# Optimization experiments

Hardware: AMD Instinct MI355X
Metric: run time of the kernel (lower is better)

The kernel has to match this reference:

```python
import jax, jax.numpy as jnp
import numpy as np

D_IN = 1024
D_OUT = 1024
NUM_HEADS = 16
HEAD_DIM = D_OUT // NUM_HEADS
SEQ = 2048
BATCH = 4


def setup_inputs() -> dict:
    key = jax.random.key(0)
    ks = jax.random.split(key, 6)
    s_in = 1.0 / np.sqrt(D_IN)
    s_out = 1.0 / np.sqrt(D_OUT)
    return {
        "inputs": jax.random.normal(ks[0], (BATCH, SEQ, D_IN), dtype=jnp.float32),
        # nn.Linear stores weight as [out, in]; y = x @ W.T
        "W_q": jax.random.uniform(ks[1], (D_OUT, D_IN), jnp.float32, -s_in, s_in),
        "W_k": jax.random.uniform(ks[2], (D_OUT, D_IN), jnp.float32, -s_in, s_in),
        "W_v": jax.random.uniform(ks[3], (D_OUT, D_IN), jnp.float32, -s_in, s_in),
        "W_o": jax.random.uniform(ks[4], (D_OUT, D_OUT), jnp.float32, -s_out, s_out),
        "b_o": jax.random.uniform(ks[5], (D_OUT,), jnp.float32, -s_out, s_out),
    }


def reference(inputs, W_q, W_k, W_v, W_o, b_o):
    B, T, _ = inputs.shape
    # projections: [B, T, d_out] -> [B, H, T, hd]
    def split_heads(x):
        return x.reshape(B, T, NUM_HEADS, HEAD_DIM).transpose(0, 2, 1, 3)

    Q = split_heads(inputs @ W_q.T)
    K = split_heads(inputs @ W_k.T)
    V = split_heads(inputs @ W_v.T)

    # [B, H, T, T] causal attention scores
    scores = jnp.einsum("bhqd,bhkd->bhqk", Q, K)
    causal = jnp.tril(jnp.ones((T, T), dtype=bool))  # True = keep
    scores = jnp.where(causal, scores, -jnp.inf)
    weights = jax.nn.softmax(scores / np.sqrt(HEAD_DIM), axis=-1)
    # dropout p=0.0 (eval mode): identity

    ctx = jnp.einsum("bhqk,bhkd->bhqd", weights, V)
    ctx = ctx.transpose(0, 2, 1, 3).reshape(B, T, D_OUT)
    return ctx @ W_o.T + b_o
```

## Files before the change

kernel.cpp:

```cpp
#include <hip/hip_runtime.h>
#include <cstdint>
#include <cstddef>

#define D_MODEL 1024
#define SEQQ    2048
#define NBATCH  4
#define NHEAD   16
#define HDIM    64
#define MTOT    (NBATCH * SEQQ)

typedef __attribute__((ext_vector_type(8))) short short8;
typedef __attribute__((ext_vector_type(4))) float floatx4;
typedef unsigned short u16;

__device__ __forceinline__ u16 f2bf(float f) {
  union { float f; uint32_t u; } a; a.f = f;
  uint32_t u = a.u;
  u += 0x7fffu + ((u >> 16) & 1u);
  return (u16)(u >> 16);
}

__device__ __forceinline__ floatx4 mfma16(short8 a, short8 b, floatx4 c) {
  return __builtin_amdgcn_mfma_f32_16x16x32_bf16(a, b, c, 0, 0, 0);
}

__device__ __forceinline__ void load_lds16(const void* g, void* l) {
  __builtin_amdgcn_global_load_lds(
      (const __attribute__((address_space(1))) uint32_t*)g,
      (__attribute__((address_space(3))) uint32_t*)l, 16, 0, 0);
}

__global__ __launch_bounds__(256) void k_cast_all(
    const float* __restrict__ X, const float* __restrict__ w0,
    const float* __restrict__ w1, const float* __restrict__ w2,
    const float* __restrict__ w3,
    u16* __restrict__ xb, u16* __restrict__ y0, u16* __restrict__ y1,
    u16* __restrict__ y2, u16* __restrict__ y3) {
  const int bx = blockIdx.x;
  const float* src; u16* dst; int i;
  if (bx < 8192) {
    src = X; dst = xb; i = (bx * 256 + threadIdx.x) * 4;
  } else {
    const int w = (bx - 8192) >> 10;
    src = (w == 0) ? w0 : (w == 1) ? w1 : (w == 2) ? w2 : w3;
    dst = (w == 0) ? y0 : (w == 1) ? y1 : (w == 2) ? y2 : y3;
    i = (((bx - 8192) & 1023) * 256 + threadIdx.x) * 4;
  }
  float4 v = *(const float4*)(src + i);
  ushort4 o;
  o.x = f2bf(v.x); o.y = f2bf(v.y); o.z = f2bf(v.z); o.w = f2bf(v.w);
  *(ushort4*)(dst + i) = o;
}

__global__ __launch_bounds__(256) void k_gemm_bt(
    const u16* __restrict__ A,
    const u16* __restrict__ B0, const u16* __restrict__ B1, const u16* __restrict__ B2,
    void* __restrict__ C0, void* __restrict__ C1, u16* __restrict__ VtOut,
    const float* __restrict__ bias, int M, int N, int K, int f32out, float ascaleQ) {
  __shared__ __align__(16) u16 As[128 * 64];
  __shared__ __align__(16) u16 Bs[128 * 64];
  const int tid = threadIdx.x;
  const int lane = tid & 63, wave = tid >> 6;
  const int quad = lane >> 4, l15 = lane & 15;
  const int m0 = blockIdx.y * 128, n0 = blockIdx.x * 128;
  const int wr = wave >> 1, wc = wave & 1;
  const u16* Bm = (blockIdx.z == 0) ? B0 : (blockIdx.z == 1 ? B1 : B2);
  void* Cm = (blockIdx.z == 0) ? C0 : C1;
  const float ascale = (blockIdx.z == 0) ? ascaleQ : 1.0f;

  floatx4 acc[4][4];
#pragma unroll
  for (int i = 0; i < 4; ++i)
#pragma unroll
    for (int j = 0; j < 4; ++j) acc[i][j] = (floatx4){0.f, 0.f, 0.f, 0.f};

  const int srow = tid >> 3;
  const int scolx = ((tid & 7) * 8) ^ ((srow & 7) * 8);
  const u16* Ag = A + (size_t)(m0 + srow) * K + scolx;
  const u16* Bg = Bm + (size_t)(n0 + srow) * K + scolx;

  for (int kt = 0; kt < K; kt += 64) {
    __syncthreads();
#pragma unroll
    for (int p = 0; p < 4; ++p) {
      load_lds16(Ag + (size_t)(p * 32) * K + kt, &As[p * 2048 + wave * 512]);
      load_lds16(Bg + (size_t)(p * 32) * K + kt, &Bs[p * 2048 + wave * 512]);
    }
    __syncthreads();

    short8 af[2][4], bfg[2][4];
#pragma unroll
    for (int ks = 0; ks < 2; ++ks) {
      const int kkx = (ks * 32 + quad * 8) ^ ((l15 & 7) * 8);
#pragma unroll
      for (int i = 0; i < 4; ++i) {
        af[ks][i]  = *(const short8*)&As[(wr * 64 + i * 16 + l15) * 64 + kkx];
        bfg[ks][i] = *(const short8*)&Bs[(wc * 64 + i * 16 + l15) * 64 + kkx];
      }
    }
#pragma unroll
    for (int ks = 0; ks < 2; ++ks)
#pragma unroll
      for (int mi = 0; mi < 4; ++mi)
#pragma unroll
        for (int ni = 0; ni < 4; ++ni)
          acc[mi][ni] = mfma16(af[ks][mi], bfg[ks][ni], acc[mi][ni]);
  }

  if (blockIdx.z == 2) {
#pragma unroll
    for (int mi = 0; mi < 4; ++mi) {
#pragma unroll
      for (int ni = 0; ni < 4; ++ni) {
        const int row = m0 + wr * 64 + mi * 16 + quad * 4;
        const int col = n0 + wc * 64 + ni * 16 + l15;
        const int b = row >> 11, t = row & 2047;
        const int h = col >> 6, d = col & 63;
        ushort4 pk;
        pk.x = f2bf(acc[mi][ni][0]); pk.y = f2bf(acc[mi][ni][1]);
        pk.z = f2bf(acc[mi][ni][2]); pk.w = f2bf(acc[mi][ni][3]);
        *(ushort4*)(VtOut + (((size_t)(b * 16 + h) * 64 + d) * SEQQ + t)) = pk;
      }
    }
    return;
  }
#pragma unroll
  for (int mi = 0; mi < 4; ++mi) {
#pragma unroll
    for (int ni = 0; ni < 4; ++ni) {
      const int row = m0 + wr * 64 + mi * 16 + quad * 4;
      const int col = n0 + wc * 64 + ni * 16 + l15;
      const float bv = bias ? bias[col] : 0.f;
#pragma unroll
      for (int r = 0; r < 4; ++r) {
        const float v = acc[mi][ni][r] * ascale + bv;
        if (f32out) ((float*)Cm)[(size_t)(row + r) * N + col] = v;
        else        ((u16*)Cm)[(size_t)(row + r) * N + col] = f2bf(v);
      }
    }
  }
}

__device__ __forceinline__ void softmax_pack(
    floatx4 (&st)[4], float& lp, u16* psw, int quad, int l15) {
#pragma unroll
  for (int ni = 0; ni < 4; ++ni) {
    const float p0 = __builtin_amdgcn_exp2f(st[ni][0]);
    const float p1 = __builtin_amdgcn_exp2f(st[ni][1]);
    const float p2 = __builtin_amdgcn_exp2f(st[ni][2]);
    const float p3 = __builtin_amdgcn_exp2f(st[ni][3]);
    lp += (p0 + p1) + (p2 + p3);
    uint2 pk;
    pk.x = __builtin_amdgcn_perm(__float_as_uint(p1), __float_as_uint(p0), 0x07060302u);
    pk.y = __builtin_amdgcn_perm(__float_as_uint(p3), __float_as_uint(p2), 0x07060302u);
    *(uint2*)&psw[l15 * 64 + ((ni * 16 + quad * 4) ^ ((l15 & 7) * 8))] = pk;
  }
}

__device__ __forceinline__ void pv_mfma(
    floatx4 (&acc)[4], const u16* psw, const short8 (&vf)[2][4], int quad, int l15) {
#pragma unroll
  for (int kc = 0; kc < 2; ++kc) {
    const short8 pf = *(const short8*)&psw[l15 * 64 +
                                           ((kc * 32 + quad * 8) ^ ((l15 & 7) * 8))];
#pragma unroll
    for (int di = 0; di < 4; ++di)
      acc[di] = mfma16(pf, vf[kc][di], acc[di]);
  }
}

__global__ __launch_bounds__(256) void k_attn(
    const u16* __restrict__ Q, const u16* __restrict__ Kg,
    const u16* __restrict__ Vt, u16* __restrict__ O) {
  __shared__ __align__(16) u16 Ks[2][64 * 64];
  __shared__ __align__(16) u16 Vs[2][64 * 64];
  __shared__ __align__(16) u16 Ps[4][2][16 * 64];
  const int tid = threadIdx.x, lane = tid & 63, wave = tid >> 6;
  const int quad = lane >> 4, l15 = lane & 15;

  const int lin = blockIdx.x;
  const int kgrp = lin >> 8, c = lin & 255;
  const int a = c & 7;
  const int p = (kgrp & 1) ? (15 - a) : a;
  const int bh = ((c >> 3) << 1) | (kgrp >> 1);
  const int b = bh >> 4, h = bh & 15;

  const int qwA = 64 * p + wave * 16;
  const int qwB = SEQQ - 64 * (p + 1) + wave * 16;
  const int nT = 32 - p;

  const u16* kbase = Kg + (size_t)(b * SEQQ) * D_MODEL + h * HDIM;
  const u16* vbase = Vt + (size_t)bh * (HDIM * SEQQ);

  const int srow = tid >> 3;
  const int scol = ((tid & 7) * 8) ^ ((srow & 7) * 8);

  {
    load_lds16(kbase + (size_t)srow * D_MODEL + scol,        &Ks[0][wave * 512]);
    load_lds16(kbase + (size_t)(32 + srow) * D_MODEL + scol, &Ks[0][2048 + wave * 512]);
    load_lds16(vbase + (size_t)srow * SEQQ + scol,           &Vs[0][wave * 512]);
    load_lds16(vbase + (size_t)(32 + srow) * SEQQ + scol,    &Vs[0][2048 + wave * 512]);
  }

  short8 qfA[2], qfB[2];
  {
    const u16* qa = Q + (size_t)(b * SEQQ + qwA + l15) * D_MODEL + h * HDIM;
    const u16* qb = Q + (size_t)(b * SEQQ + qwB + l15) * D_MODEL + h * HDIM;
#pragma unroll
    for (int ks = 0; ks < 2; ++ks) {
      qfA[ks] = *(const short8*)(qa + ks * 32 + quad * 8);
      qfB[ks] = *(const short8*)(qb + ks * 32 + quad * 8);
    }
  }

  floatx4 accA[4], accB[4];
  float lAp = 0.f, lBp = 0.f;
#pragma unroll
  for (int i = 0; i < 4; ++i) {
    accA[i] = (floatx4){0.f, 0.f, 0.f, 0.f};
    accB[i] = (floatx4){0.f, 0.f, 0.f, 0.f};
  }

  u16* pswA = &Ps[wave][0][0];
  u16* pswB = &Ps[wave][1][0];

  for (int t = 0; t < nT; ++t) {
    const int cur = t & 1;
    __syncthreads();
    if (t + 1 < nT) {
      const int kt1 = (t + 1) * 64, nxt = cur ^ 1;
      load_lds16(kbase + (size_t)(kt1 + srow) * D_MODEL + scol,      &Ks[nxt][wave * 512]);
      load_lds16(kbase + (size_t)(kt1 + 32 + srow) * D_MODEL + scol, &Ks[nxt][2048 + wave * 512]);
      load_lds16(vbase + (size_t)srow * SEQQ + kt1 + scol,           &Vs[nxt][wave * 512]);
      load_lds16(vbase + (size_t)(32 + srow) * SEQQ + kt1 + scol,    &Vs[nxt][2048 + wave * 512]);
    }
    const int kt = t * 64;

    short8 kf[4][2];
#pragma unroll
    for (int ni = 0; ni < 4; ++ni)
#pragma unroll
      for (int ks = 0; ks < 2; ++ks)
        kf[ni][ks] = *(const short8*)&Ks[cur][(ni * 16 + l15) * 64 +
                                            ((ks * 32 + quad * 8) ^ ((l15 & 7) * 8))];
    short8 vf[2][4];
#pragma unroll
    for (int kc = 0; kc < 2; ++kc)
#pragma unroll
      for (int di = 0; di < 4; ++di)
        vf[kc][di] = *(const short8*)&Vs[cur][(di * 16 + l15) * 64 +
                                             ((kc * 32 + quad * 8) ^ ((l15 & 7) * 8))];

    const bool doA = (t <= p);
    if (doA) {
      floatx4 st[4];
#pragma unroll
      for (int ni = 0; ni < 4; ++ni) {
        floatx4 s = (floatx4){0.f, 0.f, 0.f, 0.f};
        s = mfma16(kf[ni][0], qfA[0], s);
        s = mfma16(kf[ni][1], qfA[1], s);
        st[ni] = s;
      }
      if (t == p) {
        const int qg = qwA + l15;
#pragma unroll
        for (int ni = 0; ni < 4; ++ni) {
          const int kg = kt + ni * 16 + quad * 4;
#pragma unroll
          for (int r = 0; r < 4; ++r)
            if (kg + r > qg) st[ni][r] = -1e30f;
        }
      }
      softmax_pack(st, lAp, pswA, quad, l15);
    }
    {
      floatx4 st[4];
#pragma unroll
      for (int ni = 0; ni < 4; ++ni) {
        floatx4 s = (floatx4){0.f, 0.f, 0.f, 0.f};
        s = mfma16(kf[ni][0], qfB[0], s);
        s = mfma16(kf[ni][1], qfB[1], s);
        st[ni] = s;
      }
      if (t == nT - 1) {
        const int qg = qwB + l15;
#pragma unroll
        for (int ni = 0; ni < 4; ++ni) {
          const int kg = kt + ni * 16 + quad * 4;
#pragma unroll
          for (int r = 0; r < 4; ++r)
            if (kg + r > qg) st[ni][r] = -1e30f;
        }
      }
      softmax_pack(st, lBp, pswB, quad, l15);
    }
    asm volatile("s_waitcnt lgkmcnt(0)" ::: "memory");
    if (doA) pv_mfma(accA, pswA, vf, quad, l15);
    pv_mfma(accB, pswB, vf, quad, l15);
  }

  lAp += __shfl_xor(lAp, 16); lAp += __shfl_xor(lAp, 32);
  lBp += __shfl_xor(lBp, 16); lBp += __shfl_xor(lBp, 32);

  {
    u16* orow = O + (size_t)(b * SEQQ + qwA + quad * 4) * D_MODEL + h * HDIM + l15;
#pragma unroll
    for (int r = 0; r < 4; ++r) {
      const float inv = 1.0f / __shfl(lAp, quad * 4 + r, 16);
#pragma unroll
      for (int di = 0; di < 4; ++di)
        orow[(size_t)r * D_MODEL + di * 16] = f2bf(accA[di][r] * inv);
    }
  }
  {
    u16* orow = O + (size_t)(b * SEQQ + qwB + quad * 4) * D_MODEL + h * HDIM + l15;
#pragma unroll
    for (int r = 0; r < 4; ++r) {
      const float inv = 1.0f / __shfl(lBp, quad * 4 + r, 16);
#pragma unroll
      for (int di = 0; di < 4; ++di)
        orow[(size_t)r * D_MODEL + di * 16] = f2bf(accB[di][r] * inv);
    }
  }
}

extern "C" void kernel_launch(void* const* d_in, const int* in_sizes, int n_in,
                              void* d_out, int out_size, void* d_ws, size_t ws_size,
                              hipStream_t stream) {
  const float* X  = (const float*)d_in[0];
  const float* Wq = (const float*)d_in[1];
  const float* Wk = (const float*)d_in[2];
  const float* Wv = (const float*)d_in[3];
  const float* Wo = (const float*)d_in[4];
  const float* bo = (const float*)d_in[5];
  float* out = (float*)d_out;

  u16* ws = (u16*)d_ws;
  const size_t NE = (size_t)MTOT * D_MODEL;
  u16* Xb  = ws;
  u16* Qb  = Xb + NE;
  u16* Kb  = Qb + NE;
  u16* Vt  = Kb + NE;
  u16* Cb  = Vt + NE;
  u16* Wqb = Cb + NE;
  u16* Wkb = Wqb + (size_t)D_MODEL * D_MODEL;
  u16* Wvb = Wkb + (size_t)D_MODEL * D_MODEL;
  u16* Wob = Wvb + (size_t)D_MODEL * D_MODEL;

  const float SCL2E = 0.18033688f;

  k_cast_all<<<12288, 256, 0, stream>>>(X, Wq, Wk, Wv, Wo, Xb, Wqb, Wkb, Wvb, Wob);

  k_gemm_bt<<<dim3(D_MODEL / 128, MTOT / 128, 3), 256, 0, stream>>>(
      Xb, Wqb, Wkb, Wvb, Qb, Kb, Vt, nullptr, MTOT, D_MODEL, D_MODEL, 0, SCL2E);

  k_attn<<<1024, 256, 0, stream>>>(Qb, Kb, Vt, Cb);

  k_gemm_bt<<<dim3(D_MODEL / 128, MTOT / 128, 1), 256, 0, stream>>>(
      Cb, Wob, Wob, Wob, out, out, nullptr, bo, MTOT, D_MODEL, D_MODEL, 1, 1.0f);
}
```

Before: 273.1 us.

## Merge two query-tile pairs per attention block to share K/V tiles across 8 waves

The attention kernel now launches 512 blocks of 512 threads instead of 1024 blocks of 256. Each block's two wave groups handle adjacent query-tile pairs (a=2g and 2g+1) while sharing one stream of K/V tiles loaded into LDS. Each thread now loads one K and one V row chunk per tile instead of two, which is meant to halve global K/V traffic per query row and reduce loads per thread. The B-side tile is now guarded by a per-wave-group last tile. In exchange, the wave groups are imbalanced at the causal boundary, so some waves idle on the final tiles while others still compute, and there are fewer blocks per CU.

```diff
diff --git a/kernel.cpp b/kernel.cpp
--- a/kernel.cpp
+++ b/kernel.cpp
@@ -169,25 +169,27 @@
   }
 }
 
-__global__ __launch_bounds__(256) void k_attn(
+__global__ __launch_bounds__(512) void k_attn(
     const u16* __restrict__ Q, const u16* __restrict__ Kg,
     const u16* __restrict__ Vt, u16* __restrict__ O) {
   __shared__ __align__(16) u16 Ks[2][64 * 64];
   __shared__ __align__(16) u16 Vs[2][64 * 64];
-  __shared__ __align__(16) u16 Ps[4][2][16 * 64];
+  __shared__ __align__(16) u16 Ps[8][2][16 * 64];
   const int tid = threadIdx.x, lane = tid & 63, wave = tid >> 6;
   const int quad = lane >> 4, l15 = lane & 15;
 
   const int lin = blockIdx.x;
-  const int kgrp = lin >> 8, c = lin & 255;
-  const int a = c & 7;
-  const int p = (kgrp & 1) ? (15 - a) : a;
-  const int bh = ((c >> 3) << 1) | (kgrp >> 1);
+  const int c = lin & 255, k2 = lin >> 8;
+  const int g = k2 ? (7 - (c & 7)) : (c & 7);
+  const int bh = (c >> 3) | (k2 << 5);
   const int b = bh >> 4, h = bh & 15;
 
-  const int qwA = 64 * p + wave * 16;
-  const int qwB = SEQQ - 64 * (p + 1) + wave * 16;
-  const int nT = 32 - p;
+  const int wgrp = wave >> 2, wsub = wave & 3;
+  const int a = 2 * g + wgrp;
+  const int qwA = 64 * a + wsub * 16;
+  const int qwB = SEQQ - 64 * (a + 1) + wsub * 16;
+  const int nT = 32 - 2 * g;
+  const int lastB = 31 - a;
 
   const u16* kbase = Kg + (size_t)(b * SEQQ) * D_MODEL + h * HDIM;
   const u16* vbase = Vt + (size_t)bh * (HDIM * SEQQ);
@@ -196,10 +198,8 @@
   const int scol = ((tid & 7) * 8) ^ ((srow & 7) * 8);
 
   {
-    load_lds16(kbase + (size_t)srow * D_MODEL + scol,        &Ks[0][wave * 512]);
-    load_lds16(kbase + (size_t)(32 + srow) * D_MODEL + scol, &Ks[0][2048 + wave * 512]);
-    load_lds16(vbase + (size_t)srow * SEQQ + scol,           &Vs[0][wave * 512]);
-    load_lds16(vbase + (size_t)(32 + srow) * SEQQ + scol,    &Vs[0][2048 + wave * 512]);
+    load_lds16(kbase + (size_t)srow * D_MODEL + scol, &Ks[0][wave * 512]);
+    load_lds16(vbase + (size_t)srow * SEQQ + scol,    &Vs[0][wave * 512]);
   }
 
   short8 qfA[2], qfB[2];
@@ -229,10 +229,8 @@
     __syncthreads();
     if (t + 1 < nT) {
       const int kt1 = (t + 1) * 64, nxt = cur ^ 1;
-      load_lds16(kbase + (size_t)(kt1 + srow) * D_MODEL + scol,      &Ks[nxt][wave * 512]);
-      load_lds16(kbase + (size_t)(kt1 + 32 + srow) * D_MODEL + scol, &Ks[nxt][2048 + wave * 512]);
-      load_lds16(vbase + (size_t)srow * SEQQ + kt1 + scol,           &Vs[nxt][wave * 512]);
-      load_lds16(vbase + (size_t)(32 + srow) * SEQQ + kt1 + scol,    &Vs[nxt][2048 + wave * 512]);
+      load_lds16(kbase + (size_t)(kt1 + srow) * D_MODEL + scol, &Ks[nxt][wave * 512]);
+      load_lds16(vbase + (size_t)srow * SEQQ + kt1 + scol,      &Vs[nxt][wave * 512]);
     }
     const int kt = t * 64;
 
@@ -251,7 +249,8 @@
         vf[kc][di] = *(const short8*)&Vs[cur][(di * 16 + l15) * 64 +
                                              ((kc * 32 + quad * 8) ^ ((l15 & 7) * 8))];
 
-    const bool doA = (t <= p);
+    const bool doA = (t <= a);
+    const bool doB = (t <= lastB);
     if (doA) {
       floatx4 st[4];
 #pragma unroll
@@ -261,7 +260,7 @@
         s = mfma16(kf[ni][1], qfA[1], s);
         st[ni] = s;
       }
-      if (t == p) {
+      if (t == a) {
         const int qg = qwA + l15;
 #pragma unroll
         for (int ni = 0; ni < 4; ++ni) {
@@ -273,7 +272,7 @@
       }
       softmax_pack(st, lAp, pswA, quad, l15);
     }
-    {
+    if (doB) {
       floatx4 st[4];
 #pragma unroll
       for (int ni = 0; ni < 4; ++ni) {
@@ -282,7 +281,7 @@
         s = mfma16(kf[ni][1], qfB[1], s);
         st[ni] = s;
       }
-      if (t == nT - 1) {
+      if (t == lastB) {
         const int qg = qwB + l15;
 #pragma unroll
         for (int ni = 0; ni < 4; ++ni) {
@@ -296,7 +295,7 @@
     }
     asm volatile("s_waitcnt lgkmcnt(0)" ::: "memory");
     if (doA) pv_mfma(accA, pswA, vf, quad, l15);
-    pv_mfma(accB, pswB, vf, quad, l15);
+    if (doB) pv_mfma(accB, pswB, vf, quad, l15);
   }
 
   lAp += __shfl_xor(lAp, 16); lAp += __shfl_xor(lAp, 32);
@@ -354,7 +353,7 @@
   k_gemm_bt<<<dim3(D_MODEL / 128, MTOT / 128, 3), 256, 0, stream>>>(
       Xb, Wqb, Wkb, Wvb, Qb, Kb, Vt, nullptr, MTOT, D_MODEL, D_MODEL, 0, SCL2E);
 
-  k_attn<<<1024, 256, 0, stream>>>(Qb, Kb, Vt, Cb);
+  k_attn<<<512, 512, 0, stream>>>(Qb, Kb, Vt, Cb);
 
   k_gemm_bt<<<dim3(D_MODEL / 128, MTOT / 128, 1), 256, 0, stream>>>(
       Cb, Wob, Wob, Wob, out, out, nullptr, bo, MTOT, D_MODEL, D_MODEL, 1, 1.0f);
```

After: 267.6 us. 2.0% less time.
